# Performance work log

Hardware: AMD Instinct MI355X
Metric: run time of the kernel (lower is better)

## Reference

```python
import jax, jax.numpy as jnp
import numpy as np

NUM_HEADS = 12
D_MODEL = 768
D_K = D_MODEL // NUM_HEADS
NEG_INF = -1e9  # matches torch masked_fill value -1000000000.0


def setup_inputs() -> dict:
    key = jax.random.key(0)
    ks = jax.random.split(key, 11)
    B, S, D = 2, 2048, D_MODEL
    s = 1.0 / np.sqrt(D)  # ~ nn.Linear default init scale
    return {
        "q": jax.random.normal(ks[0], (B, S, D), jnp.float32),
        "k": jax.random.normal(ks[1], (B, S, D), jnp.float32),
        "v": jax.random.normal(ks[2], (B, S, D), jnp.float32),
        "mask": jax.random.randint(ks[3], (B, S, S), 0, 2, jnp.int32),
        "Wq": jax.random.normal(ks[4], (D, D), jnp.float32) * s,
        "bq": jax.random.normal(ks[5], (D,), jnp.float32) * s,
        "Wk": jax.random.normal(ks[6], (D, D), jnp.float32) * s,
        "bk": jax.random.normal(ks[7], (D,), jnp.float32) * s,
        "Wv": jax.random.normal(ks[8], (D, D), jnp.float32) * s,
        "bv": jax.random.normal(ks[9], (D,), jnp.float32) * s,
    }


def reference(q, k, v, mask, Wq, bq, Wk, bk, Wv, bv):
    B, S, D = q.shape
    H, dk = NUM_HEADS, D_K
    # torch nn.Linear: x @ W.T + b, then .view(B, H, -1, d_k)
    # NOTE: source uses a raw view (NO transpose) -> plain reshape here, faithfully.
    qh = (q @ Wq.T + bq).reshape(B, H, S, dk)
    kh = (k @ Wk.T + bk).reshape(B, H, S, dk)
    vh = (v @ Wv.T + bv).reshape(B, H, S, dk)
    scores = jnp.einsum("bhqd,bhkd->bhqk", qh, kh) / jnp.sqrt(jnp.asarray(dk, q.dtype))
    # mask.unsqueeze(1): broadcast over heads; masked_fill where mask == 0
    scores = jnp.where(mask[:, None, :, :] == 0, jnp.asarray(NEG_INF, q.dtype), scores)
    attn = jax.nn.softmax(scores, axis=-1)  # dropout = identity (eval mode)
    return jnp.einsum("bhqk,bhkd->bhqd", attn, vh)  # (B, H, S, d_k); no out-proj in source
```

## Files before the change

### kernel.cpp

```cpp
#include <hip/hip_runtime.h>
#include <stdint.h>

#define NUM_B 2
#define SEQ 2048
#define DMODEL 768
#define NHEAD 12
#define DK 64
#define MROWS (NUM_B * SEQ)
#define BHS (NUM_B * NHEAD * SEQ)

typedef __attribute__((ext_vector_type(4))) float f32x4;
typedef __attribute__((ext_vector_type(16))) float f32x16;
typedef __attribute__((ext_vector_type(8))) short bf16x8;
typedef __attribute__((ext_vector_type(8))) unsigned short us8;
typedef __attribute__((ext_vector_type(4))) unsigned int u32x4;
typedef unsigned short u16;
typedef unsigned int u32;
typedef unsigned long long u64;

__device__ __forceinline__ u16 to_bf16(float f) {
  u32 u = __builtin_bit_cast(u32, f);
  u += 0x7FFFu + ((u >> 16) & 1u);
  return (u16)(u >> 16);
}

__device__ __forceinline__ u32 cvt_pk_bf16(float lo, float hi) {
  u32 r;
  asm("v_cvt_pk_bf16_f32 %0, %1, %2" : "=v"(r) : "v"(lo), "v"(hi));
  return r;
}

__device__ __forceinline__ void gload_lds16(const u16* g, u16* l) {
#pragma clang diagnostic push
#pragma clang diagnostic ignored "-Waddress-space-conversion"
  __builtin_amdgcn_global_load_lds((const __attribute__((address_space(1))) u32*)g,
                                   (__attribute__((address_space(3))) u32*)l, 16, 0, 0);
#pragma clang diagnostic pop
}

__global__ void cvt_pack(const float* s0, const float* s1, const float* s2,
                         const float* s3, const float* s4, const float* s5,
                         const int* __restrict__ mask,
                         u16* d0, u16* d1, u16* d2, u16* d3, u16* d4, u16* d5,
                         u64* __restrict__ bits, int nbig, int nsmall) {
  int y = blockIdx.y;
  if (y == 6) {
    int base = blockIdx.x * (16 * 256) + threadIdx.x;
#pragma unroll
    for (int it = 0; it < 16; ++it) {
      int i = base + it * 256;
      u64 bm = __ballot(mask[i] != 0);
      if ((threadIdx.x & 63) == 0) {
        int word = (i >> 6) & 31;
        int s = (i >> 11) & 2047;
        int b = i >> 22;
        bits[((size_t)b * 32 + word) * 2048 + s] = bm;
      }
    }
    return;
  }
  const float* src; u16* dst; int n8;
  if (y == 0)      { src = s0; dst = d0; n8 = nbig; }
  else if (y == 1) { src = s1; dst = d1; n8 = nbig; }
  else if (y == 2) { src = s2; dst = d2; n8 = nbig; }
  else if (y == 3) { src = s3; dst = d3; n8 = nsmall; }
  else if (y == 4) { src = s4; dst = d4; n8 = nsmall; }
  else             { src = s5; dst = d5; n8 = nsmall; }
  int i = blockIdx.x * blockDim.x + threadIdx.x;
  if (i >= n8) return;
  const f32x4* p = reinterpret_cast<const f32x4*>(src) + (size_t)i * 2;
  f32x4 lo = p[0], hi = p[1];
  us8 r;
  r[0] = to_bf16(lo[0]); r[1] = to_bf16(lo[1]); r[2] = to_bf16(lo[2]); r[3] = to_bf16(lo[3]);
  r[4] = to_bf16(hi[0]); r[5] = to_bf16(hi[1]); r[6] = to_bf16(hi[2]); r[7] = to_bf16(hi[3]);
  *(reinterpret_cast<us8*>(dst) + i) = r;
}

__global__ __launch_bounds__(256) void proj_gemm(
    const u16* __restrict__ X0, const u16* __restrict__ X1, const u16* __restrict__ X2,
    const u16* __restrict__ W0, const u16* __restrict__ W1, const u16* __restrict__ W2,
    const float* __restrict__ b0, const float* __restrict__ b1, const float* __restrict__ b2,
    u16* __restrict__ o0, u16* __restrict__ o1, u16* __restrict__ o2) {
  __shared__ u16 As[2][8192];
  __shared__ u16 Bs[2][8192];

  int lin = blockIdx.x + 192 * blockIdx.y;
  int wid = (lin & 7) * 72 + (lin >> 3);
  int y = wid / 192;
  int r192 = wid % 192;
  int bm = r192 / 6, bn = r192 % 6;

  const u16* X; const u16* W; const float* bias; u16* out;
  if (y == 0)      { X = X0; W = W0; bias = b0; out = o0; }
  else if (y == 1) { X = X1; W = W1; bias = b1; out = o1; }
  else             { X = X2; W = W2; bias = b2; out = o2; }
  float osc = (y == 0) ? 0.18033688011112042f : 1.0f;

  int tid = threadIdx.x, w = tid >> 6, l = tid & 63;
  int g = l >> 4, c = l & 15;
  int m0 = bm * 128, n0 = bn * 128;
  int wm = w >> 1, wn = w & 1;

  int srow = l >> 3;
  int cg = (l & 7) ^ srow;

  f32x4 acc[4][4] = {};

  auto stage = [&](int kt, int buf) {
    int k0 = kt * 64;
#pragma unroll
    for (int i = 0; i < 4; ++i) {
      int row = i * 32 + w * 8 + srow;
      gload_lds16(X + (size_t)(m0 + row) * DMODEL + k0 + cg * 8, &As[buf][(i * 256 + w * 64) * 8]);
    }
#pragma unroll
    for (int i = 0; i < 4; ++i) {
      int row = i * 32 + w * 8 + srow;
      gload_lds16(W + (size_t)(n0 + row) * DMODEL + k0 + cg * 8, &Bs[buf][(i * 256 + w * 64) * 8]);
    }
  };

  stage(0, 0);
  __syncthreads();

  for (int kt = 0; kt < 12; ++kt) {
    int cur = kt & 1;
    if (kt < 11) stage(kt + 1, cur ^ 1);
#pragma unroll
    for (int kk = 0; kk < 2; ++kk) {
      bf16x8 av[4], bv[4];
#pragma unroll
      for (int m = 0; m < 4; ++m) {
        int row = wm * 64 + m * 16 + c;
        av[m] = *(const bf16x8*)&As[cur][row * 64 + ((kk * 32 + g * 8) ^ ((row & 7) << 3))];
      }
#pragma unroll
      for (int n = 0; n < 4; ++n) {
        int row = wn * 64 + n * 16 + c;
        bv[n] = *(const bf16x8*)&Bs[cur][row * 64 + ((kk * 32 + g * 8) ^ ((row & 7) << 3))];
      }
#pragma unroll
      for (int m = 0; m < 4; ++m)
#pragma unroll
        for (int n = 0; n < 4; ++n)
          acc[m][n] = __builtin_amdgcn_mfma_f32_16x16x32_bf16(av[m], bv[n], acc[m][n], 0, 0, 0);
    }
    __syncthreads();
  }
#pragma unroll
  for (int n = 0; n < 4; ++n) {
    int gcol = n0 + wn * 64 + n * 16 + c;
    float bvv = bias[gcol];
#pragma unroll
    for (int m = 0; m < 4; ++m) {
      int grow0 = m0 + wm * 64 + m * 16 + g * 4;
#pragma unroll
      for (int r = 0; r < 4; ++r)
        out[(size_t)(grow0 + r) * DMODEL + gcol] = to_bf16((acc[m][n][r] + bvv) * osc);
    }
  }
}

__global__ __launch_bounds__(256) void transposeV(const u16* __restrict__ vh,
                                                  u16* __restrict__ vhT) {
  __shared__ u16 T[64][72];
  int bh = blockIdx.y;
  int s0 = blockIdx.x * 64;
  int tid = threadIdx.x;
#pragma unroll
  for (int it = 0; it < 2; ++it) {
    int cch = it * 256 + tid;
    int r = cch >> 3, dc = (cch & 7) * 8;
    us8 v = *(const us8*)(vh + ((size_t)bh * 2048 + s0 + r) * 64 + dc);
#pragma unroll
    for (int j = 0; j < 8; ++j) T[dc + j][r] = v[j];
  }
  __syncthreads();
#pragma unroll
  for (int it = 0; it < 2; ++it) {
    int cch = it * 256 + tid;
    int d = cch >> 3, sc = (cch & 7) * 8;
    us8 v = *(const us8*)&T[d][sc];
    *(us8*)(vhT + ((size_t)bh * 64 + d) * 2048 + s0 + sc) = v;
  }
}

__global__ __launch_bounds__(256) void attn32(
    const u16* __restrict__ qh, const u16* __restrict__ kh, const u16* __restrict__ vt,
    const u64* __restrict__ mbt, float* __restrict__ po0, float* __restrict__ po1,
    float* __restrict__ pl) {
  __shared__ u16 K0[4096], V0[4096], K1[4096], V1[4096];

  int tid = threadIdx.x, w = tid >> 6, l = tid & 63;
  int q = l & 31, hi = l >> 5;

  int lin = blockIdx.x + 16 * (blockIdx.y + 12 * blockIdx.z);
  int wid = (lin & 7) * 96 + (lin >> 3);
  int qb = wid & 15;
  int rest = wid >> 4;
  int h = rest % 12;
  int z = rest / 12;
  int b = z >> 1, strip = z & 1;
  int kbase = strip * 1024;
  size_t hb = (size_t)(b * NHEAD + h) * SEQ * DK;
  int qrow = qb * 128 + w * 32 + q;

  bf16x8 qf[4];
#pragma unroll
  for (int s = 0; s < 4; ++s)
    qf[s] = *(const bf16x8*)(qh + hb + (size_t)qrow * DK + s * 16 + hi * 8);

  bf16x8 ones;
#pragma unroll
  for (int j = 0; j < 8; ++j) ones[j] = (short)0x3F80;

  f32x16 o0 = {}, o1 = {}, o_l = {};

  int idx0 = w * 64 + l;
  int r0s = idx0 >> 3;
  int sc0 = ((idx0 & 7) ^ (r0s & 7)) * 8;
  const u16* kS = kh + hb + (size_t)(kbase + r0s) * DK + sc0;
  const u16* vS = vt + hb + (size_t)r0s * SEQ + kbase + sc0;
  const u64* mp = mbt + ((size_t)b * 32 + strip * 16) * SEQ + qrow;

  auto stage = [&](int t, u16* Kd, u16* Vd) {
    const u16* kp = kS + (size_t)t * (64 * DK);
    const u16* vp = vS + t * 64;
    gload_lds16(kp,            Kd + w * 512);
    gload_lds16(kp + 32 * DK,  Kd + 2048 + w * 512);
    gload_lds16(vp,            Vd + w * 512);
    gload_lds16(vp + 32 * SEQ, Vd + 2048 + w * 512);
  };

  int ofA[4];
#pragma unroll
  for (int s = 0; s < 4; ++s)
    ofA[s] = q * 64 + (((2 * s + hi) ^ (q & 7)) * 8);

  auto compute = [&](const u16* Kc, const u16* Vc, u64 mcur) {
    f32x16 s0 = {}, s1 = {};
    __builtin_amdgcn_s_setprio(1);
#pragma unroll
    for (int s = 0; s < 4; ++s) {
      bf16x8 k0 = *(const bf16x8*)(Kc + ofA[s]);
      bf16x8 k1 = *(const bf16x8*)(Kc + ofA[s] + 2048);
      s0 = __builtin_amdgcn_mfma_f32_32x32x16_bf16(k0, qf[s], s0, 0, 0, 0);
      s1 = __builtin_amdgcn_mfma_f32_32x32x16_bf16(k1, qf[s], s1, 0, 0, 0);
    }
    __builtin_amdgcn_s_setprio(0);

    u32 mm0 = (u32)(mcur >> (4 * hi));
    u32 mm1 = (u32)((mcur >> 32) >> (4 * hi));
#pragma unroll
    for (int r = 0; r < 16; ++r) {
      const int p = (r & 3) + 8 * (r >> 2);
      float e0 = exp2f(s0[r]);
      float e1 = exp2f(s1[r]);
      int k0m = ((int)(mm0 << (31 - p))) >> 31;
      int k1m = ((int)(mm1 << (31 - p))) >> 31;
      s0[r] = __builtin_bit_cast(float, __builtin_bit_cast(int, e0) & k0m);
      s1[r] = __builtin_bit_cast(float, __builtin_bit_cast(int, e1) & k1m);
    }

#pragma unroll
    for (int kb = 0; kb < 2; ++kb) {
#pragma unroll
      for (int hf = 0; hf < 2; ++hf) {
        int ks = kb * 2 + hf;
        u32 A0, A1, B0, B1;
        if (kb == 0) {
          A0 = cvt_pk_bf16(s0[8 * hf + 0], s0[8 * hf + 1]);
          A1 = cvt_pk_bf16(s0[8 * hf + 2], s0[8 * hf + 3]);
          B0 = cvt_pk_bf16(s0[8 * hf + 4], s0[8 * hf + 5]);
          B1 = cvt_pk_bf16(s0[8 * hf + 6], s0[8 * hf + 7]);
        } else {
          A0 = cvt_pk_bf16(s1[8 * hf + 0], s1[8 * hf + 1]);
          A1 = cvt_pk_bf16(s1[8 * hf + 2], s1[8 * hf + 3]);
          B0 = cvt_pk_bf16(s1[8 * hf + 4], s1[8 * hf + 5]);
          B1 = cvt_pk_bf16(s1[8 * hf + 6], s1[8 * hf + 7]);
        }
        asm("v_permlane32_swap_b32 %0, %1" : "+v"(A0), "+v"(B0));
        asm("v_permlane32_swap_b32 %0, %1" : "+v"(A1), "+v"(B1));
        u32x4 fw;
        fw[0] = A0; fw[1] = A1; fw[2] = B0; fw[3] = B1;
        bf16x8 pa = __builtin_bit_cast(bf16x8, fw);
        bf16x8 v0 = *(const bf16x8*)(Vc + ofA[ks]);
        bf16x8 v1 = *(const bf16x8*)(Vc + ofA[ks] + 2048);
        __builtin_amdgcn_s_setprio(1);
        o0 = __builtin_amdgcn_mfma_f32_32x32x16_bf16(pa, v0, o0, 0, 0, 0);
        o1 = __builtin_amdgcn_mfma_f32_32x32x16_bf16(pa, v1, o1, 0, 0, 0);
        o_l = __builtin_amdgcn_mfma_f32_32x32x16_bf16(pa, ones, o_l, 0, 0, 0);
        __builtin_amdgcn_s_setprio(0);
      }
    }
  };

  stage(0, K0, V0);
  u64 mcur = mp[0];
  __syncthreads();

  for (int tt = 0; tt < 8; ++tt) {
    const int t0 = 2 * tt;
    u64 mnext = mp[(size_t)(t0 + 1) * SEQ];
    stage(t0 + 1, K1, V1);
    compute(K0, V0, mcur);
    __syncthreads();
    mcur = mnext;
    if (tt < 7) {
      mnext = mp[(size_t)(t0 + 2) * SEQ];
      stage(t0 + 2, K0, V0);
    }
    compute(K1, V1, mcur);
    __syncthreads();
    mcur = mnext;
  }

  float* oo = strip ? po1 : po0;
#pragma unroll
  for (int r = 0; r < 16; ++r) {
    int row = qb * 128 + w * 32 + (r & 3) + 8 * (r >> 2) + 4 * hi;
    oo[hb + (size_t)row * DK + q]      = o0[r];
    oo[hb + (size_t)row * DK + 32 + q] = o1[r];
  }
  if (q == 0) {
    size_t base2 = (size_t)(b * NHEAD + h) * SEQ + qb * 128 + w * 32 + 4 * hi;
#pragma unroll
    for (int r = 0; r < 16; ++r)
      pl[(size_t)strip * BHS + base2 + (r & 3) + 8 * (r >> 2)] = o_l[r];
  }
}

__global__ __launch_bounds__(256) void combine_kernel(
    const float* __restrict__ po0, const float* __restrict__ po1,
    const float* __restrict__ pl, float* __restrict__ out) {
  int i = blockIdx.x * 256 + threadIdx.x;
  int row = i >> 4;
  float l0 = pl[row], l1 = pl[BHS + row];
  float inv = 1.f / (l0 + l1);
  f32x4 a = ((const f32x4*)po0)[i];
  f32x4 b = ((const f32x4*)po1)[i];
  ((f32x4*)out)[i] = (a + b) * inv;
}

extern "C" void kernel_launch(void* const* d_in, const int* in_sizes, int n_in,
                              void* d_out, int out_size, void* d_ws, size_t ws_size,
                              hipStream_t stream) {
  const float* q    = (const float*)d_in[0];
  const float* k    = (const float*)d_in[1];
  const float* v    = (const float*)d_in[2];
  const int*   mask = (const int*)d_in[3];
  const float* Wq   = (const float*)d_in[4];
  const float* bq   = (const float*)d_in[5];
  const float* Wk   = (const float*)d_in[6];
  const float* bk   = (const float*)d_in[7];
  const float* Wv   = (const float*)d_in[8];
  const float* bv   = (const float*)d_in[9];

  char* ws = (char*)d_ws;
  const size_t szX = (size_t)MROWS * DMODEL * 2;
  const size_t szW = (size_t)DMODEL * DMODEL * 2;
  u16* xq  = (u16*)(ws);
  u16* xk  = (u16*)(ws + szX);
  u16* xv  = (u16*)(ws + 2 * szX);
  u16* wqb = (u16*)(ws + 3 * szX);
  u16* wkb = (u16*)(ws + 3 * szX + szW);
  u16* wvb = (u16*)(ws + 3 * szX + 2 * szW);
  u16* qh  = (u16*)(ws + 3 * szX + 3 * szW);
  u16* kh  = (u16*)(ws + 4 * szX + 3 * szW);
  u16* vh  = (u16*)(ws + 5 * szX + 3 * szW);
  u64* mb  = (u64*)(ws + 6 * szX + 3 * szW);

  float* po1 = (float*)(ws);
  u16*   vhT = (u16*)(ws + 2 * szX);
  float* pl  = (float*)(ws + 3 * szX);
  float* po0 = (float*)d_out;

  const int nbig = (MROWS * DMODEL) / 8;
  const int nsmall = (DMODEL * DMODEL) / 8;

  cvt_pack<<<dim3(2048, 7), 256, 0, stream>>>(q, k, v, Wq, Wk, Wv, mask,
                                              xq, xk, xv, wqb, wkb, wvb, mb,
                                              nbig, nsmall);
  proj_gemm<<<dim3(192, 3), 256, 0, stream>>>(
      xq, xk, xv, wqb, wkb, wvb, bq, bk, bv, qh, kh, vh);
  transposeV<<<dim3(32, 24), 256, 0, stream>>>(vh, vhT);
  attn32<<<dim3(16, 12, 4), 256, 0, stream>>>(qh, kh, vhT, mb, po0, po1, pl);
  combine_kernel<<<(BHS * 16) / 256, 256, 0, stream>>>(po0, po1, pl, (float*)d_out);
}
```

Baseline: 116.6 us.

## Split attention key range into four strips with bf16 normalized partials

The attention kernel now splits the key sequence into four strips of 512 instead of two strips of 1024, doubling the grid so more blocks are available to fill the GPU. Each strip normalizes its own partial output by its local row sum. Three of the partials are stored as bf16 to cut write and read traffic. The combine kernel reweights the four partials by their row sums. This adds per-block overhead (Q loads, epilogue stores) and loses some precision in the bf16 partials.

```diff
diff --git a/kernel.cpp b/kernel.cpp
--- a/kernel.cpp
+++ b/kernel.cpp
@@ -13,6 +13,7 @@
 typedef __attribute__((ext_vector_type(16))) float f32x16;
 typedef __attribute__((ext_vector_type(8))) short bf16x8;
 typedef __attribute__((ext_vector_type(8))) unsigned short us8;
+typedef __attribute__((ext_vector_type(4))) unsigned short us4;
 typedef __attribute__((ext_vector_type(4))) unsigned int u32x4;
 typedef unsigned short u16;
 typedef unsigned int u32;
@@ -22,6 +23,10 @@
   u32 u = __builtin_bit_cast(u32, f);
   u += 0x7FFFu + ((u >> 16) & 1u);
   return (u16)(u >> 16);
+}
+
+__device__ __forceinline__ float bf16_to_f32(u16 u) {
+  return __builtin_bit_cast(float, ((u32)u) << 16);
 }
 
 __device__ __forceinline__ u32 cvt_pk_bf16(float lo, float hi) {
@@ -187,21 +192,21 @@
 
 __global__ __launch_bounds__(256) void attn32(
     const u16* __restrict__ qh, const u16* __restrict__ kh, const u16* __restrict__ vt,
-    const u64* __restrict__ mbt, float* __restrict__ po0, float* __restrict__ po1,
-    float* __restrict__ pl) {
+    const u64* __restrict__ mbt, float* __restrict__ po0, u16* __restrict__ po1,
+    u16* __restrict__ po2, u16* __restrict__ po3, float* __restrict__ pl) {
   __shared__ u16 K0[4096], V0[4096], K1[4096], V1[4096];
 
   int tid = threadIdx.x, w = tid >> 6, l = tid & 63;
   int q = l & 31, hi = l >> 5;
 
   int lin = blockIdx.x + 16 * (blockIdx.y + 12 * blockIdx.z);
-  int wid = (lin & 7) * 96 + (lin >> 3);
+  int wid = (lin & 7) * 192 + (lin >> 3);
   int qb = wid & 15;
   int rest = wid >> 4;
   int h = rest % 12;
   int z = rest / 12;
-  int b = z >> 1, strip = z & 1;
-  int kbase = strip * 1024;
+  int strip = z & 3, b = z >> 2;
+  int kbase = strip * 512;
   size_t hb = (size_t)(b * NHEAD + h) * SEQ * DK;
   int qrow = qb * 128 + w * 32 + q;
 
@@ -221,7 +226,7 @@
   int sc0 = ((idx0 & 7) ^ (r0s & 7)) * 8;
   const u16* kS = kh + hb + (size_t)(kbase + r0s) * DK + sc0;
   const u16* vS = vt + hb + (size_t)r0s * SEQ + kbase + sc0;
-  const u64* mp = mbt + ((size_t)b * 32 + strip * 16) * SEQ + qrow;
+  const u64* mp = mbt + ((size_t)b * 32 + strip * 8) * SEQ + qrow;
 
   auto stage = [&](int t, u16* Kd, u16* Vd) {
     const u16* kp = kS + (size_t)t * (64 * DK);
@@ -299,14 +304,14 @@
   u64 mcur = mp[0];
   __syncthreads();
 
-  for (int tt = 0; tt < 8; ++tt) {
+  for (int tt = 0; tt < 4; ++tt) {
     const int t0 = 2 * tt;
     u64 mnext = mp[(size_t)(t0 + 1) * SEQ];
     stage(t0 + 1, K1, V1);
     compute(K0, V0, mcur);
     __syncthreads();
     mcur = mnext;
-    if (tt < 7) {
+    if (tt < 3) {
       mnext = mp[(size_t)(t0 + 2) * SEQ];
       stage(t0 + 2, K0, V0);
     }
@@ -315,12 +320,23 @@
     mcur = mnext;
   }
 
-  float* oo = strip ? po1 : po0;
-#pragma unroll
-  for (int r = 0; r < 16; ++r) {
-    int row = qb * 128 + w * 32 + (r & 3) + 8 * (r >> 2) + 4 * hi;
-    oo[hb + (size_t)row * DK + q]      = o0[r];
-    oo[hb + (size_t)row * DK + 32 + q] = o1[r];
+  if (strip == 0) {
+#pragma unroll
+    for (int r = 0; r < 16; ++r) {
+      float invl = __builtin_amdgcn_rcpf(o_l[r]);
+      int row = qb * 128 + w * 32 + (r & 3) + 8 * (r >> 2) + 4 * hi;
+      po0[hb + (size_t)row * DK + q]      = o0[r] * invl;
+      po0[hb + (size_t)row * DK + 32 + q] = o1[r] * invl;
+    }
+  } else {
+    u16* oo = (strip == 1) ? po1 : (strip == 2) ? po2 : po3;
+#pragma unroll
+    for (int r = 0; r < 16; ++r) {
+      float invl = __builtin_amdgcn_rcpf(o_l[r]);
+      int row = qb * 128 + w * 32 + (r & 3) + 8 * (r >> 2) + 4 * hi;
+      oo[hb + (size_t)row * DK + q]      = to_bf16(o0[r] * invl);
+      oo[hb + (size_t)row * DK + 32 + q] = to_bf16(o1[r] * invl);
+    }
   }
   if (q == 0) {
     size_t base2 = (size_t)(b * NHEAD + h) * SEQ + qb * 128 + w * 32 + 4 * hi;
@@ -331,15 +347,23 @@
 }
 
 __global__ __launch_bounds__(256) void combine_kernel(
-    const float* __restrict__ po0, const float* __restrict__ po1,
+    const float* __restrict__ po0, const u16* __restrict__ po1,
+    const u16* __restrict__ po2, const u16* __restrict__ po3,
     const float* __restrict__ pl, float* __restrict__ out) {
   int i = blockIdx.x * 256 + threadIdx.x;
   int row = i >> 4;
-  float l0 = pl[row], l1 = pl[BHS + row];
-  float inv = 1.f / (l0 + l1);
+  float l0 = pl[row], l1 = pl[BHS + row], l2 = pl[2 * BHS + row], l3 = pl[3 * BHS + row];
+  float inv = 1.f / (l0 + l1 + l2 + l3);
   f32x4 a = ((const f32x4*)po0)[i];
-  f32x4 b = ((const f32x4*)po1)[i];
-  ((f32x4*)out)[i] = (a + b) * inv;
+  us4 b1 = ((const us4*)po1)[i];
+  us4 b2 = ((const us4*)po2)[i];
+  us4 b3 = ((const us4*)po3)[i];
+  f32x4 acc;
+#pragma unroll
+  for (int j = 0; j < 4; ++j)
+    acc[j] = a[j] * l0 + bf16_to_f32(b1[j]) * l1 + bf16_to_f32(b2[j]) * l2 +
+             bf16_to_f32(b3[j]) * l3;
+  ((f32x4*)out)[i] = acc * inv;
 }
 
 extern "C" void kernel_launch(void* const* d_in, const int* in_sizes, int n_in,
@@ -370,10 +394,12 @@
   u16* vh  = (u16*)(ws + 5 * szX + 3 * szW);
   u64* mb  = (u64*)(ws + 6 * szX + 3 * szW);
 
-  float* po1 = (float*)(ws);
-  u16*   vhT = (u16*)(ws + 2 * szX);
-  float* pl  = (float*)(ws + 3 * szX);
-  float* po0 = (float*)d_out;
+  u16*   po1b = (u16*)(ws);
+  u16*   po2b = (u16*)(ws + szX);
+  u16*   vhT  = (u16*)(ws + 2 * szX);
+  float* pl   = (float*)(ws + 3 * szX);
+  u16*   po3b = (u16*)(ws + 5 * szX + 3 * szW);
+  float* po0  = (float*)d_out;
 
   const int nbig = (MROWS * DMODEL) / 8;
   const int nsmall = (DMODEL * DMODEL) / 8;
@@ -384,6 +410,6 @@
   proj_gemm<<<dim3(192, 3), 256, 0, stream>>>(
       xq, xk, xv, wqb, wkb, wvb, bq, bk, bv, qh, kh, vh);
   transposeV<<<dim3(32, 24), 256, 0, stream>>>(vh, vhT);
-  attn32<<<dim3(16, 12, 4), 256, 0, stream>>>(qh, kh, vhT, mb, po0, po1, pl);
-  combine_kernel<<<(BHS * 16) / 256, 256, 0, stream>>>(po0, po1, pl, (float*)d_out);
-}
+  attn32<<<dim3(16, 12, 8), 256, 0, stream>>>(qh, kh, vhT, mb, po0, po1b, po2b, po3b, pl);
+  combine_kernel<<<(BHS * 16) / 256, 256, 0, stream>>>(po0, po1b, po2b, po3b, pl, (float*)d_out);
+}
```

Result: no change. 116.9 us (+0.2%).
